# Kernel optimization log

Measured on AMD Instinct MI355X. Metric: run time of the kernel, lower is better.

Reference implementation:

```python
import jax, jax.numpy as jnp
import numpy as np

SPARSITY = 0.9  # target fraction of zeros (magnitude pruning)
D_IN = 4096
D_OUT = 4096
TOKENS = 4096


def setup_inputs() -> dict:
    key = jax.random.key(0)
    k1, k2 = jax.random.split(key)
    x = jax.random.normal(k1, (TOKENS, D_IN), dtype=jnp.float32)
    weight = jax.random.normal(k2, (D_OUT, D_IN), dtype=jnp.float32) * 0.01
    bias = jnp.zeros((D_OUT,), dtype=jnp.float32)
    return {"x": x, "weight": weight, "bias": bias}


def reference(x, weight, bias):
    # Magnitude pruning: threshold at the SPARSITY quantile of |W|,
    # keep only entries strictly above threshold (matches CSR build),
    # then sparse-dense GEMM y = x @ W_pruned^T + b.
    aw = jnp.abs(weight)
    thr = jnp.quantile(aw, SPARSITY)
    w_pruned = jnp.where(aw > thr, weight, jnp.zeros_like(weight))
    return x @ w_pruned.T + bias
```

## Files before the change

### kernel.cpp

```cpp
#include <hip/hip_runtime.h>
#include <stdint.h>

#define D_IN   4096
#define D_OUT  4096
#define NTOK   4096
#define NW     (D_OUT * D_IN)
#define RANK1  15099493u
#define CAP    1500000

typedef unsigned int  uint32;
typedef unsigned short ushort_t;
typedef float  f32x4  __attribute__((ext_vector_type(4)));
typedef __bf16 bf16x8 __attribute__((ext_vector_type(8)));

__device__ __forceinline__ uint32 rne_bf16(float f) {
  uint32 u = __float_as_uint(f);
  return (u + 0x7FFFu + ((u >> 16) & 1u)) >> 16;
}

__device__ __forceinline__ void gload_lds16(const void* g, void* l) {
  __builtin_amdgcn_global_load_lds((__attribute__((address_space(1))) void*)(g),
                                   (__attribute__((address_space(3))) void*)(l), 16, 0, 0);
}

template <int NB>
__device__ __forceinline__ void dsel(const uint32* __restrict__ h, uint32 rank,
                                     uint32* res, uint32* wtot) {
  constexpr int PER = NB >> 8;
  int tid = threadIdx.x;
  int lane = tid & 63, wid = tid >> 6;
  uint32 loc[PER];
  uint32 s = 0;
  int base = tid * PER;
#pragma unroll
  for (int i = 0; i < PER; i++) { loc[i] = h[base + i]; s += loc[i]; }
  uint32 v = s;
  for (int d = 1; d < 64; d <<= 1) { uint32 o = __shfl_up(v, (unsigned)d); if (lane >= d) v += o; }
  if (lane == 63) wtot[wid] = v;
  __syncthreads();
  uint32 woff = 0;
  for (int w = 0; w < wid; w++) woff += wtot[w];
  uint32 incl = v + woff, excl = incl - s;
  if (rank >= excl && rank < incl) {
    uint32 c = excl;
#pragma unroll
    for (int i = 0; i < PER; i++) {
      if (rank < c + loc[i]) { res[0] = (uint32)(base + i); res[1] = rank - c; break; }
      c += loc[i];
    }
  }
  __syncthreads();
}

__global__ void k1_hist1_convx(const uint4* __restrict__ wb, uint32* __restrict__ hist,
                               const float4* __restrict__ x, uint4* __restrict__ xout) {
  __shared__ uint32 lh[4][2048];
  if (blockIdx.x < 2048) {
    for (int i = threadIdx.x; i < 8192; i += 256) ((uint32*)lh)[i] = 0;
    __syncthreads();
    int wid = threadIdx.x >> 6;
    int idx = blockIdx.x * 256 + threadIdx.x;
    for (int i = idx; i < NW / 4; i += 2048 * 256) {
      uint4 v = wb[i];
      atomicAdd(&lh[wid][(v.x & 0x7FFFFFFFu) >> 20], 1u);
      atomicAdd(&lh[wid][(v.y & 0x7FFFFFFFu) >> 20], 1u);
      atomicAdd(&lh[wid][(v.z & 0x7FFFFFFFu) >> 20], 1u);
      atomicAdd(&lh[wid][(v.w & 0x7FFFFFFFu) >> 20], 1u);
    }
    __syncthreads();
    for (int i = threadIdx.x; i < 2048; i += 256) {
      uint32 c = lh[0][i] + lh[1][i] + lh[2][i] + lh[3][i];
      if (c) atomicAdd(&hist[i], c);
    }
  } else {
    int i = (blockIdx.x - 2048) * 256 + threadIdx.x;
    for (; i < NW / 8; i += 1024 * 256) {
      float4 a = x[2 * i], b = x[2 * i + 1];
      uint4 o;
      o.x = rne_bf16(a.x) | (rne_bf16(a.y) << 16);
      o.y = rne_bf16(a.z) | (rne_bf16(a.w) << 16);
      o.z = rne_bf16(b.x) | (rne_bf16(b.y) << 16);
      o.w = rne_bf16(b.z) | (rne_bf16(b.w) << 16);
      xout[i] = o;
    }
  }
}

__global__ void k2_decide(const float4* __restrict__ w, const uint32* __restrict__ hist1,
                          uint4* __restrict__ out, uint2* __restrict__ cand,
                          uint32* __restrict__ cnt) {
  __shared__ uint32 res1[2], wt[4];
  __shared__ uint32 lcnt, lbase;
  __shared__ uint2 lbuf[3072];
  if (threadIdx.x == 0) lcnt = 0;
  dsel<2048>(hist1, RANK1, res1, wt);
  uint32 bstar = res1[0];
  int i = blockIdx.x * 256 + threadIdx.x;
  for (; i < NW / 8; i += 512 * 256) {
    float4 a = w[2 * i], b = w[2 * i + 1];
    float f[8] = {a.x, a.y, a.z, a.w, b.x, b.y, b.z, b.w};
    uint32 h[8];
#pragma unroll
    for (int j = 0; j < 8; j++) {
      uint32 bits = __float_as_uint(f[j]);
      uint32 bin = (bits & 0x7FFFFFFFu) >> 20;
      h[j] = (bin > bstar) ? rne_bf16(f[j]) : 0u;
      if (bin == bstar) {
        uint32 p = atomicAdd(&lcnt, 1u);
        if (p < 3072) lbuf[p] = make_uint2((uint32)(8 * i + j), bits);
      }
    }
    uint4 o;
    o.x = h[0] | (h[1] << 16);
    o.y = h[2] | (h[3] << 16);
    o.z = h[4] | (h[5] << 16);
    o.w = h[6] | (h[7] << 16);
    out[i] = o;
  }
  __syncthreads();
  if (threadIdx.x == 0) lbase = atomicAdd(cnt, lcnt);
  __syncthreads();
  for (uint32 p = threadIdx.x; p < lcnt && p < 3072; p += 256) {
    uint32 g = lbase + p;
    if (g < CAP) cand[g] = lbuf[p];
  }
}

__global__ void s1_hist(const uint2* __restrict__ cand, const uint32* __restrict__ cnt,
                        uint32* __restrict__ hs1) {
  __shared__ uint32 lh[1024];
  for (int i = threadIdx.x; i < 1024; i += 256) lh[i] = 0;
  __syncthreads();
  uint32 n = *cnt; if (n > CAP) n = CAP;
  for (uint32 i = blockIdx.x * 256 + threadIdx.x; i < n; i += gridDim.x * 256) {
    uint32 mag = cand[i].y & 0x7FFFFFFFu;
    atomicAdd(&lh[(mag >> 10) & 1023u], 1u);
  }
  __syncthreads();
  for (int i = threadIdx.x; i < 1024; i += 256) if (lh[i]) atomicAdd(&hs1[i], lh[i]);
}

__global__ void s2_hist(const uint2* __restrict__ cand, const uint32* __restrict__ cnt,
                        const uint32* __restrict__ hist1, const uint32* __restrict__ hs1,
                        uint32* __restrict__ hs2) {
  __shared__ uint32 lh[1024];
  __shared__ uint32 res1[2], res2[2], wt[4];
  for (int i = threadIdx.x; i < 1024; i += 256) lh[i] = 0;
  dsel<2048>(hist1, RANK1, res1, wt);
  dsel<1024>(hs1, res1[1], res2, wt);
  uint32 b2 = res2[0];
  uint32 n = *cnt; if (n > CAP) n = CAP;
  for (uint32 i = blockIdx.x * 256 + threadIdx.x; i < n; i += gridDim.x * 256) {
    uint32 mag = cand[i].y & 0x7FFFFFFFu;
    if (((mag >> 10) & 1023u) == b2) atomicAdd(&lh[mag & 1023u], 1u);
  }
  __syncthreads();
  for (int i = threadIdx.x; i < 1024; i += 256) if (lh[i]) atomicAdd(&hs2[i], lh[i]);
}

__global__ void k5_fixup(const uint2* __restrict__ cand, const uint32* __restrict__ cnt,
                         const uint32* __restrict__ hist1, const uint32* __restrict__ hs1,
                         const uint32* __restrict__ hs2, ushort_t* __restrict__ wb) {
  __shared__ uint32 res1[2], res2[2], res3[2], wt[4];
  dsel<2048>(hist1, RANK1, res1, wt);
  dsel<1024>(hs1, res1[1], res2, wt);
  dsel<1024>(hs2, res2[1], res3, wt);
  uint32 thr_mag = (res1[0] << 20) | (res2[0] << 10) | res3[0];
  uint32 n = *cnt; if (n > CAP) n = CAP;
  for (uint32 i = blockIdx.x * 256 + threadIdx.x; i < n; i += gridDim.x * 256) {
    uint2 c = cand[i];
    uint32 mag = c.y & 0x7FFFFFFFu;
    if (mag > thr_mag) wb[c.x] = (ushort_t)rne_bf16(__uint_as_float(c.y));
  }
}

#define TILES 128

#define MF16(AF, BF, MO)                                                                          \
  acc[(MO)+0][0] = __builtin_amdgcn_mfma_f32_16x16x32_bf16(AF[0], BF[0], acc[(MO)+0][0], 0,0,0);  \
  acc[(MO)+0][1] = __builtin_amdgcn_mfma_f32_16x16x32_bf16(AF[0], BF[1], acc[(MO)+0][1], 0,0,0);  \
  acc[(MO)+0][2] = __builtin_amdgcn_mfma_f32_16x16x32_bf16(AF[0], BF[2], acc[(MO)+0][2], 0,0,0);  \
  acc[(MO)+0][3] = __builtin_amdgcn_mfma_f32_16x16x32_bf16(AF[0], BF[3], acc[(MO)+0][3], 0,0,0);  \
  acc[(MO)+1][0] = __builtin_amdgcn_mfma_f32_16x16x32_bf16(AF[1], BF[0], acc[(MO)+1][0], 0,0,0);  \
  acc[(MO)+1][1] = __builtin_amdgcn_mfma_f32_16x16x32_bf16(AF[1], BF[1], acc[(MO)+1][1], 0,0,0);  \
  acc[(MO)+1][2] = __builtin_amdgcn_mfma_f32_16x16x32_bf16(AF[1], BF[2], acc[(MO)+1][2], 0,0,0);  \
  acc[(MO)+1][3] = __builtin_amdgcn_mfma_f32_16x16x32_bf16(AF[1], BF[3], acc[(MO)+1][3], 0,0,0);  \
  acc[(MO)+2][0] = __builtin_amdgcn_mfma_f32_16x16x32_bf16(AF[2], BF[0], acc[(MO)+2][0], 0,0,0);  \
  acc[(MO)+2][1] = __builtin_amdgcn_mfma_f32_16x16x32_bf16(AF[2], BF[1], acc[(MO)+2][1], 0,0,0);  \
  acc[(MO)+2][2] = __builtin_amdgcn_mfma_f32_16x16x32_bf16(AF[2], BF[2], acc[(MO)+2][2], 0,0,0);  \
  acc[(MO)+2][3] = __builtin_amdgcn_mfma_f32_16x16x32_bf16(AF[2], BF[3], acc[(MO)+2][3], 0,0,0);  \
  acc[(MO)+3][0] = __builtin_amdgcn_mfma_f32_16x16x32_bf16(AF[3], BF[0], acc[(MO)+3][0], 0,0,0);  \
  acc[(MO)+3][1] = __builtin_amdgcn_mfma_f32_16x16x32_bf16(AF[3], BF[1], acc[(MO)+3][1], 0,0,0);  \
  acc[(MO)+3][2] = __builtin_amdgcn_mfma_f32_16x16x32_bf16(AF[3], BF[2], acc[(MO)+3][2], 0,0,0);  \
  acc[(MO)+3][3] = __builtin_amdgcn_mfma_f32_16x16x32_bf16(AF[3], BF[3], acc[(MO)+3][3], 0,0,0);

#define GBODY(T, S, SN)                                                        \
  {                                                                            \
    const bf16x8* A8n = (const bf16x8*)(lds + (((T) + 1) & 3) * 16384);        \
    const bf16x8* B8n = A8n + 1024;                                            \
    bv[SN][0]  = B8n[(br +  0) * 4 + csel];                                    \
    bv[SN][1]  = B8n[(br + 16) * 4 + csel];                                    \
    bv[SN][2]  = B8n[(br + 32) * 4 + csel];                                    \
    bv[SN][3]  = B8n[(br + 48) * 4 + csel];                                    \
    a03[SN][0] = A8n[(ar +  0) * 4 + csel];                                    \
    a03[SN][1] = A8n[(ar + 16) * 4 + csel];                                    \
    a03[SN][2] = A8n[(ar + 32) * 4 + csel];                                    \
    a03[SN][3] = A8n[(ar + 48) * 4 + csel];                                    \
    __builtin_amdgcn_sched_barrier(0);                                         \
    ushort_t* sb = lds + (((T) + 3) & 3) * 16384;                              \
    gload_lds16(pA0, sb + ld0);                                                \
    gload_lds16(pA1, sb + ld1);                                                \
    gload_lds16(pB0, sb + 8192 + ld0);                                         \
    gload_lds16(pB1, sb + 8192 + ld1);                                         \
    __builtin_amdgcn_sched_barrier(0);                                         \
    asm volatile("s_waitcnt lgkmcnt(8)" ::: "memory");                         \
    __builtin_amdgcn_sched_barrier(0);                                         \
    __builtin_amdgcn_s_setprio(1);                                             \
    MF16(a47[S], bv[S], 4)                                                     \
    __builtin_amdgcn_s_setprio(0);                                             \
    __builtin_amdgcn_sched_barrier(0);                                         \
    a47[SN][0] = A8n[(ar +  64) * 4 + csel];                                   \
    a47[SN][1] = A8n[(ar +  80) * 4 + csel];                                   \
    a47[SN][2] = A8n[(ar +  96) * 4 + csel];                                   \
    a47[SN][3] = A8n[(ar + 112) * 4 + csel];                                   \
    __builtin_amdgcn_sched_barrier(0);                                         \
    asm volatile("s_waitcnt lgkmcnt(4)" ::: "memory");                         \
    asm volatile("s_waitcnt vmcnt(4)" ::: "memory");                           \
    asm volatile("s_barrier" ::: "memory");                                    \
    __builtin_amdgcn_sched_barrier(0);                                         \
    __builtin_amdgcn_s_setprio(1);                                             \
    MF16(a03[SN], bv[SN], 0)                                                   \
    __builtin_amdgcn_s_setprio(0);                                             \
    __builtin_amdgcn_sched_barrier(0);                                         \
    if ((T) < TILES - 4) { pA0 += 32; pA1 += 32; pB0 += 32; pB1 += 32; }       \
  }

__global__ __launch_bounds__(512, 2) void gemm_bt(const ushort_t* __restrict__ A,
                                                  const ushort_t* __restrict__ B,
                                                  const float* __restrict__ bias,
                                                  float* __restrict__ C) {
  extern __shared__ ushort_t lds[];

  int bid = blockIdx.x;
  int swz = (bid & 7) * 32 + (bid >> 3);
  int bm = swz >> 4;
  int bn = swz & 15;

  int tid  = threadIdx.x;
  int lane = tid & 63;
  int wave = tid >> 6;
  int wm = wave >> 2, wn = wave & 3;

  int l15  = lane & 15;
  int csel = (lane >> 4) ^ ((lane >> 1) & 3);

  int idx0 = tid, idx1 = 512 + tid;
  int sr0 = idx0 >> 2, scl0 = (idx0 & 3) ^ ((sr0 >> 1) & 3);
  int sr1 = idx1 >> 2, scl1 = (idx1 & 3) ^ ((sr1 >> 1) & 3);
  int ld0 = idx0 * 8, ld1 = idx1 * 8;
  const ushort_t* pA0 = A + (size_t)(bm * 256 + sr0) * D_IN + scl0 * 8;
  const ushort_t* pA1 = A + (size_t)(bm * 256 + sr1) * D_IN + scl1 * 8;
  const ushort_t* pB0 = B + (size_t)(bn * 256 + sr0) * D_IN + scl0 * 8;
  const ushort_t* pB1 = B + (size_t)(bn * 256 + sr1) * D_IN + scl1 * 8;

  f32x4 acc[8][4];
#pragma unroll
  for (int m = 0; m < 8; m++)
#pragma unroll
    for (int n = 0; n < 4; n++) acc[m][n] = (f32x4){0.f, 0.f, 0.f, 0.f};

  gload_lds16(pA0,      lds + ld0);         gload_lds16(pA1,      lds + ld1);
  gload_lds16(pB0,      lds + 8192 + ld0);  gload_lds16(pB1,      lds + 8192 + ld1);
  gload_lds16(pA0 + 32, lds + 16384 + ld0); gload_lds16(pA1 + 32, lds + 16384 + ld1);
  gload_lds16(pB0 + 32, lds + 24576 + ld0); gload_lds16(pB1 + 32, lds + 24576 + ld1);
  gload_lds16(pA0 + 64, lds + 32768 + ld0); gload_lds16(pA1 + 64, lds + 32768 + ld1);
  gload_lds16(pB0 + 64, lds + 40960 + ld0); gload_lds16(pB1 + 64, lds + 40960 + ld1);
  pA0 += 96; pA1 += 96; pB0 += 96; pB1 += 96;
  asm volatile("s_waitcnt vmcnt(4)" ::: "memory");
  asm volatile("s_barrier" ::: "memory");

  int ar = wm * 128 + l15;
  int br = wn * 64 + l15;

  bf16x8 bv[2][4], a03[2][4], a47[2][4];

  {
    const bf16x8* A8 = (const bf16x8*)lds;
    const bf16x8* B8 = A8 + 1024;
    bv[0][0]  = B8[(br +  0) * 4 + csel];
    bv[0][1]  = B8[(br + 16) * 4 + csel];
    bv[0][2]  = B8[(br + 32) * 4 + csel];
    bv[0][3]  = B8[(br + 48) * 4 + csel];
    a03[0][0] = A8[(ar +  0) * 4 + csel];
    a03[0][1] = A8[(ar + 16) * 4 + csel];
    a03[0][2] = A8[(ar + 32) * 4 + csel];
    a03[0][3] = A8[(ar + 48) * 4 + csel];
    __builtin_amdgcn_sched_barrier(0);
    a47[0][0] = A8[(ar +  64) * 4 + csel];
    a47[0][1] = A8[(ar +  80) * 4 + csel];
    a47[0][2] = A8[(ar +  96) * 4 + csel];
    a47[0][3] = A8[(ar + 112) * 4 + csel];
    __builtin_amdgcn_sched_barrier(0);
    asm volatile("s_waitcnt lgkmcnt(4)" ::: "memory");
    __builtin_amdgcn_sched_barrier(0);
    __builtin_amdgcn_s_setprio(1);
    MF16(a03[0], bv[0], 0)
    __builtin_amdgcn_s_setprio(0);
    __builtin_amdgcn_sched_barrier(0);
  }

  for (int tt = 0; tt < 63; tt++) {
    int t0 = tt * 2;
    GBODY(t0, 0, 1)
    GBODY(t0 + 1, 1, 0)
  }
  GBODY(126, 0, 1)

  asm volatile("s_waitcnt lgkmcnt(0)" ::: "memory");
  __builtin_amdgcn_sched_barrier(0);
  __builtin_amdgcn_s_setprio(1);
  MF16(a47[1], bv[1], 4)
  __builtin_amdgcn_s_setprio(0);

  int orow0 = bm * 256 + wm * 128 + (lane >> 4) * 4;
  int ocol0 = bn * 256 + wn * 64 + l15;
#pragma unroll
  for (int n = 0; n < 4; n++) {
    float bb = bias[ocol0 + n * 16];
#pragma unroll
    for (int m = 0; m < 8; m++) {
#pragma unroll
      for (int r = 0; r < 4; r++) {
        C[(size_t)(orow0 + m * 16 + r) * D_OUT + ocol0 + n * 16] = acc[m][n][r] + bb;
      }
    }
  }
}

extern "C" void kernel_launch(void* const* d_in, const int* in_sizes, int n_in,
                              void* d_out, int out_size, void* d_ws, size_t ws_size,
                              hipStream_t stream) {
  const float* x = (const float*)d_in[0];
  const float* w = (const float*)d_in[1];
  const float* bias = (const float*)d_in[2];
  float* out = (float*)d_out;

  char* ws = (char*)d_ws;
  uint32* hist1 = (uint32*)ws;
  uint32* hs1   = (uint32*)(ws + 8192);
  uint32* hs2   = (uint32*)(ws + 12288);
  uint32* cnt   = (uint32*)(ws + 16384);
  ushort_t* Xb  = (ushort_t*)(ws + 65536);
  ushort_t* Wb  = (ushort_t*)(ws + 65536 + (size_t)NW * 2);
  uint2*   cand = (uint2*)(ws + 65536 + (size_t)NW * 4);

  hipMemsetAsync(d_ws, 0, 16448, stream);

  k1_hist1_convx<<<3072, 256, 0, stream>>>((const uint4*)w, hist1, (const float4*)x, (uint4*)Xb);
  k2_decide<<<512, 256, 0, stream>>>((const float4*)w, hist1, (uint4*)Wb, cand, cnt);
  s1_hist<<<128, 256, 0, stream>>>(cand, cnt, hs1);
  s2_hist<<<128, 256, 0, stream>>>(cand, cnt, hist1, hs1, hs2);
  k5_fixup<<<256, 256, 0, stream>>>(cand, cnt, hist1, hs1, hs2, Wb);

  gemm_bt<<<256, 512, 131072, stream>>>(Xb, Wb, bias, out);
}
```

Before: 212.5 us.

## Load B fragments directly from global into registers, stage only A in LDS

```diff
diff --git a/kernel.cpp b/kernel.cpp
--- a/kernel.cpp
+++ b/kernel.cpp
@@ -194,45 +194,51 @@
   acc[(MO)+3][2] = __builtin_amdgcn_mfma_f32_16x16x32_bf16(AF[3], BF[2], acc[(MO)+3][2], 0,0,0);  \
   acc[(MO)+3][3] = __builtin_amdgcn_mfma_f32_16x16x32_bf16(AF[3], BF[3], acc[(MO)+3][3], 0,0,0);
 
-#define GBODY(T, S, SN)                                                        \
+#define GBODY2(T, S, SN)                                                       \
   {                                                                            \
-    const bf16x8* A8n = (const bf16x8*)(lds + (((T) + 1) & 3) * 16384);        \
-    const bf16x8* B8n = A8n + 1024;                                            \
-    bv[SN][0]  = B8n[(br +  0) * 4 + csel];                                    \
-    bv[SN][1]  = B8n[(br + 16) * 4 + csel];                                    \
-    bv[SN][2]  = B8n[(br + 32) * 4 + csel];                                    \
-    bv[SN][3]  = B8n[(br + 48) * 4 + csel];                                    \
+                                     \
+    bq[SN][0] = *(const bf16x8*)pB0v;                                          \
+    bq[SN][1] = *(const bf16x8*)pB1v;                                          \
+    bq[SN][2] = *(const bf16x8*)pB2v;                                          \
+    bq[SN][3] = *(const bf16x8*)pB3v;                                          \
+    __builtin_amdgcn_sched_barrier(0);                                         \
+                                                  \
+    ushort_t* sb = lds + (((T) + 2) & 3) * 8192;                               \
+    gload_lds16(pA0, sb + ld0);                                                \
+    gload_lds16(pA1, sb + ld1);                                                \
+    __builtin_amdgcn_sched_barrier(0);                                         \
+                                                             \
+    const bf16x8* A8c = (const bf16x8*)(lds + ((T) & 3) * 8192);               \
+    a47[0] = A8c[(ar +  64) * 4 + csel];                                       \
+    a47[1] = A8c[(ar +  80) * 4 + csel];                                       \
+    a47[2] = A8c[(ar +  96) * 4 + csel];                                       \
+    a47[3] = A8c[(ar + 112) * 4 + csel];                                       \
+    __builtin_amdgcn_sched_barrier(0);                                         \
+    asm volatile("s_waitcnt lgkmcnt(4)" ::: "memory");      \
+    __builtin_amdgcn_sched_barrier(0);                                         \
+    __builtin_amdgcn_s_setprio(1);                                             \
+    MF16(a03[S], bq[S], 0)                                                     \
+    __builtin_amdgcn_s_setprio(0);                                             \
+    __builtin_amdgcn_sched_barrier(0);                                         \
+    asm volatile("s_waitcnt lgkmcnt(0)" ::: "memory");      \
+    __builtin_amdgcn_sched_barrier(0);                                         \
+    __builtin_amdgcn_s_setprio(1);                                             \
+    MF16(a47, bq[S], 4)                                                        \
+    __builtin_amdgcn_s_setprio(0);                                             \
+    __builtin_amdgcn_sched_barrier(0);                                         \
+                        \
+    asm volatile("s_waitcnt vmcnt(2)" ::: "memory");                           \
+    __builtin_amdgcn_sched_barrier(0);                                         \
+                                     \
+    const bf16x8* A8n = (const bf16x8*)(lds + (((T) + 1) & 3) * 8192);         \
     a03[SN][0] = A8n[(ar +  0) * 4 + csel];                                    \
     a03[SN][1] = A8n[(ar + 16) * 4 + csel];                                    \
     a03[SN][2] = A8n[(ar + 32) * 4 + csel];                                    \
     a03[SN][3] = A8n[(ar + 48) * 4 + csel];                                    \
     __builtin_amdgcn_sched_barrier(0);                                         \
-    ushort_t* sb = lds + (((T) + 3) & 3) * 16384;                              \
-    gload_lds16(pA0, sb + ld0);                                                \
-    gload_lds16(pA1, sb + ld1);                                                \
-    gload_lds16(pB0, sb + 8192 + ld0);                                         \
-    gload_lds16(pB1, sb + 8192 + ld1);                                         \
-    __builtin_amdgcn_sched_barrier(0);                                         \
-    asm volatile("s_waitcnt lgkmcnt(8)" ::: "memory");                         \
-    __builtin_amdgcn_sched_barrier(0);                                         \
-    __builtin_amdgcn_s_setprio(1);                                             \
-    MF16(a47[S], bv[S], 4)                                                     \
-    __builtin_amdgcn_s_setprio(0);                                             \
-    __builtin_amdgcn_sched_barrier(0);                                         \
-    a47[SN][0] = A8n[(ar +  64) * 4 + csel];                                   \
-    a47[SN][1] = A8n[(ar +  80) * 4 + csel];                                   \
-    a47[SN][2] = A8n[(ar +  96) * 4 + csel];                                   \
-    a47[SN][3] = A8n[(ar + 112) * 4 + csel];                                   \
-    __builtin_amdgcn_sched_barrier(0);                                         \
-    asm volatile("s_waitcnt lgkmcnt(4)" ::: "memory");                         \
-    asm volatile("s_waitcnt vmcnt(4)" ::: "memory");                           \
     asm volatile("s_barrier" ::: "memory");                                    \
-    __builtin_amdgcn_sched_barrier(0);                                         \
-    __builtin_amdgcn_s_setprio(1);                                             \
-    MF16(a03[SN], bv[SN], 0)                                                   \
-    __builtin_amdgcn_s_setprio(0);                                             \
-    __builtin_amdgcn_sched_barrier(0);                                         \
-    if ((T) < TILES - 4) { pA0 += 32; pA1 += 32; pB0 += 32; pB1 += 32; }       \
+    if ((T) < TILES - 3) { pA0 += 32; pA1 += 32; }                             \
+    if ((T) < TILES - 2) { pB0v += 32; pB1v += 32; pB2v += 32; pB3v += 32; }   \
   }
 
 __global__ __launch_bounds__(512, 2) void gemm_bt(const ushort_t* __restrict__ A,
@@ -252,7 +258,8 @@
   int wm = wave >> 2, wn = wave & 3;
 
   int l15  = lane & 15;
-  int csel = (lane >> 4) ^ ((lane >> 1) & 3);
+  int kq   = lane >> 4;
+  int csel = kq ^ ((lane >> 1) & 3);
 
   int idx0 = tid, idx1 = 512 + tid;
   int sr0 = idx0 >> 2, scl0 = (idx0 & 3) ^ ((sr0 >> 1) & 3);
@@ -260,8 +267,12 @@
   int ld0 = idx0 * 8, ld1 = idx1 * 8;
   const ushort_t* pA0 = A + (size_t)(bm * 256 + sr0) * D_IN + scl0 * 8;
   const ushort_t* pA1 = A + (size_t)(bm * 256 + sr1) * D_IN + scl1 * 8;
-  const ushort_t* pB0 = B + (size_t)(bn * 256 + sr0) * D_IN + scl0 * 8;
-  const ushort_t* pB1 = B + (size_t)(bn * 256 + sr1) * D_IN + scl1 * 8;
+
+  int brow = bn * 256 + wn * 64 + l15;
+  const ushort_t* pB0v = B + (size_t)(brow +  0) * D_IN + kq * 8 + 32;
+  const ushort_t* pB1v = B + (size_t)(brow + 16) * D_IN + kq * 8 + 32;
+  const ushort_t* pB2v = B + (size_t)(brow + 32) * D_IN + kq * 8 + 32;
+  const ushort_t* pB3v = B + (size_t)(brow + 48) * D_IN + kq * 8 + 32;
 
   f32x4 acc[8][4];
 #pragma unroll
@@ -269,58 +280,58 @@
 #pragma unroll
     for (int n = 0; n < 4; n++) acc[m][n] = (f32x4){0.f, 0.f, 0.f, 0.f};
 
-  gload_lds16(pA0,      lds + ld0);         gload_lds16(pA1,      lds + ld1);
-  gload_lds16(pB0,      lds + 8192 + ld0);  gload_lds16(pB1,      lds + 8192 + ld1);
-  gload_lds16(pA0 + 32, lds + 16384 + ld0); gload_lds16(pA1 + 32, lds + 16384 + ld1);
-  gload_lds16(pB0 + 32, lds + 24576 + ld0); gload_lds16(pB1 + 32, lds + 24576 + ld1);
-  gload_lds16(pA0 + 64, lds + 32768 + ld0); gload_lds16(pA1 + 64, lds + 32768 + ld1);
-  gload_lds16(pB0 + 64, lds + 40960 + ld0); gload_lds16(pB1 + 64, lds + 40960 + ld1);
-  pA0 += 96; pA1 += 96; pB0 += 96; pB1 += 96;
-  asm volatile("s_waitcnt vmcnt(4)" ::: "memory");
+  bf16x8 bq[2][4], a03[2][4], a47[4];
+
+  gload_lds16(pA0, lds + ld0);
+  gload_lds16(pA1, lds + ld1);
+  __builtin_amdgcn_sched_barrier(0);
+  bq[0][0] = *(const bf16x8*)(pB0v - 32);
+  bq[0][1] = *(const bf16x8*)(pB1v - 32);
+  bq[0][2] = *(const bf16x8*)(pB2v - 32);
+  bq[0][3] = *(const bf16x8*)(pB3v - 32);
+  __builtin_amdgcn_sched_barrier(0);
+  gload_lds16(pA0 + 32, lds + 8192 + ld0);
+  gload_lds16(pA1 + 32, lds + 8192 + ld1);
+  pA0 += 64; pA1 += 64;
+  __builtin_amdgcn_sched_barrier(0);
+  asm volatile("s_waitcnt vmcnt(2)" ::: "memory");
   asm volatile("s_barrier" ::: "memory");
 
   int ar = wm * 128 + l15;
-  int br = wn * 64 + l15;
-
-  bf16x8 bv[2][4], a03[2][4], a47[2][4];
 
   {
     const bf16x8* A8 = (const bf16x8*)lds;
-    const bf16x8* B8 = A8 + 1024;
-    bv[0][0]  = B8[(br +  0) * 4 + csel];
-    bv[0][1]  = B8[(br + 16) * 4 + csel];
-    bv[0][2]  = B8[(br + 32) * 4 + csel];
-    bv[0][3]  = B8[(br + 48) * 4 + csel];
     a03[0][0] = A8[(ar +  0) * 4 + csel];
     a03[0][1] = A8[(ar + 16) * 4 + csel];
     a03[0][2] = A8[(ar + 32) * 4 + csel];
     a03[0][3] = A8[(ar + 48) * 4 + csel];
     __builtin_amdgcn_sched_barrier(0);
-    a47[0][0] = A8[(ar +  64) * 4 + csel];
-    a47[0][1] = A8[(ar +  80) * 4 + csel];
-    a47[0][2] = A8[(ar +  96) * 4 + csel];
-    a47[0][3] = A8[(ar + 112) * 4 + csel];
+  }
+
+  for (int tt = 0; tt < 63; tt++) {
+    GBODY2(2 * tt,     0, 1)
+    GBODY2(2 * tt + 1, 1, 0)
+  }
+  GBODY2(126, 0, 1)
+
+  {
+    const bf16x8* A8c = (const bf16x8*)(lds + (127 & 3) * 8192);
+    a47[0] = A8c[(ar +  64) * 4 + csel];
+    a47[1] = A8c[(ar +  80) * 4 + csel];
+    a47[2] = A8c[(ar +  96) * 4 + csel];
+    a47[3] = A8c[(ar + 112) * 4 + csel];
     __builtin_amdgcn_sched_barrier(0);
     asm volatile("s_waitcnt lgkmcnt(4)" ::: "memory");
     __builtin_amdgcn_sched_barrier(0);
     __builtin_amdgcn_s_setprio(1);
-    MF16(a03[0], bv[0], 0)
+    MF16(a03[1], bq[1], 0)
     __builtin_amdgcn_s_setprio(0);
+    asm volatile("s_waitcnt lgkmcnt(0)" ::: "memory");
     __builtin_amdgcn_sched_barrier(0);
-  }
-
-  for (int tt = 0; tt < 63; tt++) {
-    int t0 = tt * 2;
-    GBODY(t0, 0, 1)
-    GBODY(t0 + 1, 1, 0)
-  }
-  GBODY(126, 0, 1)
-
-  asm volatile("s_waitcnt lgkmcnt(0)" ::: "memory");
-  __builtin_amdgcn_sched_barrier(0);
-  __builtin_amdgcn_s_setprio(1);
-  MF16(a47[1], bv[1], 4)
-  __builtin_amdgcn_s_setprio(0);
+    __builtin_amdgcn_s_setprio(1);
+    MF16(a47, bq[1], 4)
+    __builtin_amdgcn_s_setprio(0);
+  }
 
   int orow0 = bm * 256 + wm * 128 + (lane >> 4) * 4;
   int ocol0 = bn * 256 + wn * 64 + l15;
@@ -362,5 +373,5 @@
   s2_hist<<<128, 256, 0, stream>>>(cand, cnt, hist1, hs1, hs2);
   k5_fixup<<<256, 256, 0, stream>>>(cand, cnt, hist1, hs1, hs2, Wb);
 
-  gemm_bt<<<256, 512, 131072, stream>>>(Xb, Wb, bias, out);
-}
+  gemm_bt<<<256, 512, 65536, stream>>>(Xb, Wb, bias, out);
+}
```

Result: slower. 293.0 us (+37.9%).

## Fuse pruning prep kernels into one persistent kernel with grid barriers

Applied to the files above, without the earlier changes.

```diff
diff --git a/kernel.cpp b/kernel.cpp
--- a/kernel.cpp
+++ b/kernel.cpp
@@ -7,6 +7,7 @@
 #define NW     (D_OUT * D_IN)
 #define RANK1  15099493u
 #define CAP    1500000
+#define PREPB  1024
 
 typedef unsigned int  uint32;
 typedef unsigned short ushort_t;
@@ -23,9 +24,21 @@
                                    (__attribute__((address_space(3))) void*)(l), 16, 0, 0);
 }
 
+__device__ __forceinline__ void gridbar(uint32* bar, uint32 target) {
+  __syncthreads();
+  __threadfence();
+  if (threadIdx.x == 0) {
+    __hip_atomic_fetch_add(bar, 1u, __ATOMIC_RELAXED, __HIP_MEMORY_SCOPE_AGENT);
+    while (__hip_atomic_load(bar, __ATOMIC_RELAXED, __HIP_MEMORY_SCOPE_AGENT) < target)
+      __builtin_amdgcn_s_sleep(8);
+  }
+  __syncthreads();
+  __threadfence();
+}
+
 template <int NB>
 __device__ __forceinline__ void dsel(const uint32* __restrict__ h, uint32 rank,
-                                     uint32* res, uint32* wtot) {
+                                     volatile uint32* res, volatile uint32* wtot) {
   constexpr int PER = NB >> 8;
   int tid = threadIdx.x;
   int lane = tid & 63, wid = tid >> 6;
@@ -52,29 +65,34 @@
   __syncthreads();
 }
 
-__global__ void k1_hist1_convx(const uint4* __restrict__ wb, uint32* __restrict__ hist,
-                               const float4* __restrict__ x, uint4* __restrict__ xout) {
-  __shared__ uint32 lh[4][2048];
-  if (blockIdx.x < 2048) {
-    for (int i = threadIdx.x; i < 8192; i += 256) ((uint32*)lh)[i] = 0;
-    __syncthreads();
-    int wid = threadIdx.x >> 6;
-    int idx = blockIdx.x * 256 + threadIdx.x;
-    for (int i = idx; i < NW / 4; i += 2048 * 256) {
-      uint4 v = wb[i];
-      atomicAdd(&lh[wid][(v.x & 0x7FFFFFFFu) >> 20], 1u);
-      atomicAdd(&lh[wid][(v.y & 0x7FFFFFFFu) >> 20], 1u);
-      atomicAdd(&lh[wid][(v.z & 0x7FFFFFFFu) >> 20], 1u);
-      atomicAdd(&lh[wid][(v.w & 0x7FFFFFFFu) >> 20], 1u);
-    }
-    __syncthreads();
-    for (int i = threadIdx.x; i < 2048; i += 256) {
-      uint32 c = lh[0][i] + lh[1][i] + lh[2][i] + lh[3][i];
-      if (c) atomicAdd(&hist[i], c);
-    }
-  } else {
-    int i = (blockIdx.x - 2048) * 256 + threadIdx.x;
-    for (; i < NW / 8; i += 1024 * 256) {
+__global__ __launch_bounds__(256, 4) void prep(const float* __restrict__ w,
+                                               const float4* __restrict__ x,
+                                               uint4* __restrict__ xout,
+                                               uint4* __restrict__ wout,
+                                               uint2* __restrict__ cand,
+                                               uint32* __restrict__ hist1,
+                                               uint32* __restrict__ hs1,
+                                               uint32* __restrict__ hs2,
+                                               uint32* __restrict__ cnt,
+                                               uint32* __restrict__ bar) {
+  __shared__ uint32 smem[8192];
+  __shared__ uint32 sres1[2], sres2[2], sres3[2], swt[4], slcnt, slbase;
+  int tid = threadIdx.x, bid = blockIdx.x;
+
+  {
+    uint32* lh = smem;
+    for (int i = tid; i < 8192; i += 256) lh[i] = 0;
+    __syncthreads();
+    int wid = tid >> 6;
+    const uint4* wb4 = (const uint4*)w;
+    for (int i = bid * 256 + tid; i < NW / 4; i += PREPB * 256) {
+      uint4 v = wb4[i];
+      atomicAdd(&lh[wid * 2048 + ((v.x & 0x7FFFFFFFu) >> 20)], 1u);
+      atomicAdd(&lh[wid * 2048 + ((v.y & 0x7FFFFFFFu) >> 20)], 1u);
+      atomicAdd(&lh[wid * 2048 + ((v.z & 0x7FFFFFFFu) >> 20)], 1u);
+      atomicAdd(&lh[wid * 2048 + ((v.w & 0x7FFFFFFFu) >> 20)], 1u);
+    }
+    for (int i = bid * 256 + tid; i < NW / 8; i += PREPB * 256) {
       float4 a = x[2 * i], b = x[2 * i + 1];
       uint4 o;
       o.x = rne_bf16(a.x) | (rne_bf16(a.y) << 16);
@@ -83,94 +101,85 @@
       o.w = rne_bf16(b.z) | (rne_bf16(b.w) << 16);
       xout[i] = o;
     }
-  }
-}
-
-__global__ void k2_decide(const float4* __restrict__ w, const uint32* __restrict__ hist1,
-                          uint4* __restrict__ out, uint2* __restrict__ cand,
-                          uint32* __restrict__ cnt) {
-  __shared__ uint32 res1[2], wt[4];
-  __shared__ uint32 lcnt, lbase;
-  __shared__ uint2 lbuf[3072];
-  if (threadIdx.x == 0) lcnt = 0;
-  dsel<2048>(hist1, RANK1, res1, wt);
-  uint32 bstar = res1[0];
-  int i = blockIdx.x * 256 + threadIdx.x;
-  for (; i < NW / 8; i += 512 * 256) {
-    float4 a = w[2 * i], b = w[2 * i + 1];
-    float f[8] = {a.x, a.y, a.z, a.w, b.x, b.y, b.z, b.w};
-    uint32 h[8];
-#pragma unroll
-    for (int j = 0; j < 8; j++) {
-      uint32 bits = __float_as_uint(f[j]);
-      uint32 bin = (bits & 0x7FFFFFFFu) >> 20;
-      h[j] = (bin > bstar) ? rne_bf16(f[j]) : 0u;
-      if (bin == bstar) {
-        uint32 p = atomicAdd(&lcnt, 1u);
-        if (p < 3072) lbuf[p] = make_uint2((uint32)(8 * i + j), bits);
+    __syncthreads();
+    for (int i = tid; i < 2048; i += 256) {
+      uint32 c = lh[i] + lh[2048 + i] + lh[4096 + i] + lh[6144 + i];
+      if (c) atomicAdd(&hist1[i], c);
+    }
+  }
+  gridbar(bar, PREPB);
+
+  {
+    uint2*  lbuf = (uint2*)smem;
+    uint32* lch  = smem + 6144;
+    for (int i = tid; i < 1024; i += 256) lch[i] = 0;
+    if (tid == 0) slcnt = 0;
+    dsel<2048>(hist1, RANK1, sres1, swt);
+    uint32 bstar = sres1[0];
+    const float4* w4 = (const float4*)w;
+    for (int i = bid * 256 + tid; i < NW / 8; i += PREPB * 256) {
+      float4 a = w4[2 * i], b = w4[2 * i + 1];
+      float f[8] = {a.x, a.y, a.z, a.w, b.x, b.y, b.z, b.w};
+      uint32 h[8];
+#pragma unroll
+      for (int j = 0; j < 8; j++) {
+        uint32 bits = __float_as_uint(f[j]);
+        uint32 bin = (bits & 0x7FFFFFFFu) >> 20;
+        h[j] = (bin > bstar) ? rne_bf16(f[j]) : 0u;
+        if (bin == bstar) {
+          uint32 p = atomicAdd(&slcnt, 1u);
+          if (p < 3072) {
+            lbuf[p] = make_uint2((uint32)(8 * i + j), bits);
+            atomicAdd(&lch[(bits >> 10) & 1023u], 1u);
+          }
+        }
       }
-    }
-    uint4 o;
-    o.x = h[0] | (h[1] << 16);
-    o.y = h[2] | (h[3] << 16);
-    o.z = h[4] | (h[5] << 16);
-    o.w = h[6] | (h[7] << 16);
-    out[i] = o;
-  }
-  __syncthreads();
-  if (threadIdx.x == 0) lbase = atomicAdd(cnt, lcnt);
-  __syncthreads();
-  for (uint32 p = threadIdx.x; p < lcnt && p < 3072; p += 256) {
-    uint32 g = lbase + p;
-    if (g < CAP) cand[g] = lbuf[p];
-  }
-}
-
-__global__ void s1_hist(const uint2* __restrict__ cand, const uint32* __restrict__ cnt,
-                        uint32* __restrict__ hs1) {
-  __shared__ uint32 lh[1024];
-  for (int i = threadIdx.x; i < 1024; i += 256) lh[i] = 0;
-  __syncthreads();
-  uint32 n = *cnt; if (n > CAP) n = CAP;
-  for (uint32 i = blockIdx.x * 256 + threadIdx.x; i < n; i += gridDim.x * 256) {
-    uint32 mag = cand[i].y & 0x7FFFFFFFu;
-    atomicAdd(&lh[(mag >> 10) & 1023u], 1u);
-  }
-  __syncthreads();
-  for (int i = threadIdx.x; i < 1024; i += 256) if (lh[i]) atomicAdd(&hs1[i], lh[i]);
-}
-
-__global__ void s2_hist(const uint2* __restrict__ cand, const uint32* __restrict__ cnt,
-                        const uint32* __restrict__ hist1, const uint32* __restrict__ hs1,
-                        uint32* __restrict__ hs2) {
-  __shared__ uint32 lh[1024];
-  __shared__ uint32 res1[2], res2[2], wt[4];
-  for (int i = threadIdx.x; i < 1024; i += 256) lh[i] = 0;
-  dsel<2048>(hist1, RANK1, res1, wt);
-  dsel<1024>(hs1, res1[1], res2, wt);
-  uint32 b2 = res2[0];
-  uint32 n = *cnt; if (n > CAP) n = CAP;
-  for (uint32 i = blockIdx.x * 256 + threadIdx.x; i < n; i += gridDim.x * 256) {
-    uint32 mag = cand[i].y & 0x7FFFFFFFu;
-    if (((mag >> 10) & 1023u) == b2) atomicAdd(&lh[mag & 1023u], 1u);
-  }
-  __syncthreads();
-  for (int i = threadIdx.x; i < 1024; i += 256) if (lh[i]) atomicAdd(&hs2[i], lh[i]);
-}
-
-__global__ void k5_fixup(const uint2* __restrict__ cand, const uint32* __restrict__ cnt,
-                         const uint32* __restrict__ hist1, const uint32* __restrict__ hs1,
-                         const uint32* __restrict__ hs2, ushort_t* __restrict__ wb) {
-  __shared__ uint32 res1[2], res2[2], res3[2], wt[4];
-  dsel<2048>(hist1, RANK1, res1, wt);
-  dsel<1024>(hs1, res1[1], res2, wt);
-  dsel<1024>(hs2, res2[1], res3, wt);
-  uint32 thr_mag = (res1[0] << 20) | (res2[0] << 10) | res3[0];
-  uint32 n = *cnt; if (n > CAP) n = CAP;
-  for (uint32 i = blockIdx.x * 256 + threadIdx.x; i < n; i += gridDim.x * 256) {
-    uint2 c = cand[i];
-    uint32 mag = c.y & 0x7FFFFFFFu;
-    if (mag > thr_mag) wb[c.x] = (ushort_t)rne_bf16(__uint_as_float(c.y));
+      uint4 o;
+      o.x = h[0] | (h[1] << 16);
+      o.y = h[2] | (h[3] << 16);
+      o.z = h[4] | (h[5] << 16);
+      o.w = h[6] | (h[7] << 16);
+      wout[i] = o;
+    }
+    __syncthreads();
+    uint32 nstore = slcnt < 3072u ? slcnt : 3072u;
+    if (tid == 0) slbase = atomicAdd(cnt, nstore);
+    __syncthreads();
+    for (uint32 p = tid; p < nstore; p += 256) {
+      uint32 g = slbase + p;
+      if (g < CAP) cand[g] = lbuf[p];
+    }
+    for (int i = tid; i < 1024; i += 256) if (lch[i]) atomicAdd(&hs1[i], lch[i]);
+  }
+  gridbar(bar, 2 * PREPB);
+
+  {
+    for (int i = tid; i < 1024; i += 256) smem[i] = 0;
+    dsel<2048>(hist1, RANK1, sres1, swt);
+    dsel<1024>(hs1, sres1[1], sres2, swt);
+    uint32 b2 = sres2[0];
+    uint32 n = *cnt; if (n > CAP) n = CAP;
+    for (uint32 i = bid * 256 + tid; i < n; i += PREPB * 256) {
+      uint32 mag = cand[i].y & 0x7FFFFFFFu;
+      if (((mag >> 10) & 1023u) == b2) atomicAdd(&smem[mag & 1023u], 1u);
+    }
+    __syncthreads();
+    for (int i = tid; i < 1024; i += 256) if (smem[i]) atomicAdd(&hs2[i], smem[i]);
+  }
+  gridbar(bar, 3 * PREPB);
+
+  {
+    dsel<2048>(hist1, RANK1, sres1, swt);
+    dsel<1024>(hs1, sres1[1], sres2, swt);
+    dsel<1024>(hs2, sres2[1], sres3, swt);
+    uint32 thr_mag = (sres1[0] << 20) | (sres2[0] << 10) | sres3[0];
+    uint32 n = *cnt; if (n > CAP) n = CAP;
+    ushort_t* wb16 = (ushort_t*)wout;
+    for (uint32 i = bid * 256 + tid; i < n; i += PREPB * 256) {
+      uint2 c = cand[i];
+      uint32 mag = c.y & 0x7FFFFFFFu;
+      if (mag > thr_mag) wb16[c.x] = (ushort_t)rne_bf16(__uint_as_float(c.y));
+    }
   }
 }
 
@@ -350,17 +359,15 @@
   uint32* hs1   = (uint32*)(ws + 8192);
   uint32* hs2   = (uint32*)(ws + 12288);
   uint32* cnt   = (uint32*)(ws + 16384);
+  uint32* bar   = (uint32*)(ws + 16388);
   ushort_t* Xb  = (ushort_t*)(ws + 65536);
   ushort_t* Wb  = (ushort_t*)(ws + 65536 + (size_t)NW * 2);
   uint2*   cand = (uint2*)(ws + 65536 + (size_t)NW * 4);
 
   hipMemsetAsync(d_ws, 0, 16448, stream);
 
-  k1_hist1_convx<<<3072, 256, 0, stream>>>((const uint4*)w, hist1, (const float4*)x, (uint4*)Xb);
-  k2_decide<<<512, 256, 0, stream>>>((const float4*)w, hist1, (uint4*)Wb, cand, cnt);
-  s1_hist<<<128, 256, 0, stream>>>(cand, cnt, hs1);
-  s2_hist<<<128, 256, 0, stream>>>(cand, cnt, hist1, hs1, hs2);
-  k5_fixup<<<256, 256, 0, stream>>>(cand, cnt, hist1, hs1, hs2, Wb);
+  prep<<<PREPB, 256, 0, stream>>>(w, (const float4*)x, (uint4*)Xb, (uint4*)Wb,
+                                  cand, hist1, hs1, hs2, cnt, bar);
 
   gemm_bt<<<256, 512, 131072, stream>>>(Xb, Wb, bias, out);
 }
```

Result: slower. 778.0 us (+266.1%).

## Fuse candidate histogram into decide kernel and restructure GEMM as paired-tile double buffer

Applied to the files above, without the earlier changes.

```diff
diff --git a/kernel.cpp b/kernel.cpp
--- a/kernel.cpp
+++ b/kernel.cpp
@@ -88,10 +88,12 @@
 
 __global__ void k2_decide(const float4* __restrict__ w, const uint32* __restrict__ hist1,
                           uint4* __restrict__ out, uint2* __restrict__ cand,
-                          uint32* __restrict__ cnt) {
+                          uint32* __restrict__ cnt, uint32* __restrict__ hs1) {
   __shared__ uint32 res1[2], wt[4];
   __shared__ uint32 lcnt, lbase;
   __shared__ uint2 lbuf[3072];
+  __shared__ uint32 lch[1024];
+  for (int i = threadIdx.x; i < 1024; i += 256) lch[i] = 0;
   if (threadIdx.x == 0) lcnt = 0;
   dsel<2048>(hist1, RANK1, res1, wt);
   uint32 bstar = res1[0];
@@ -107,7 +109,10 @@
       h[j] = (bin > bstar) ? rne_bf16(f[j]) : 0u;
       if (bin == bstar) {
         uint32 p = atomicAdd(&lcnt, 1u);
-        if (p < 3072) lbuf[p] = make_uint2((uint32)(8 * i + j), bits);
+        if (p < 3072) {
+          lbuf[p] = make_uint2((uint32)(8 * i + j), bits);
+          atomicAdd(&lch[(bits >> 10) & 1023u], 1u);
+        }
       }
     }
     uint4 o;
@@ -118,26 +123,14 @@
     out[i] = o;
   }
   __syncthreads();
-  if (threadIdx.x == 0) lbase = atomicAdd(cnt, lcnt);
-  __syncthreads();
-  for (uint32 p = threadIdx.x; p < lcnt && p < 3072; p += 256) {
+  uint32 nstore = lcnt < 3072u ? lcnt : 3072u;
+  if (threadIdx.x == 0) lbase = atomicAdd(cnt, nstore);
+  __syncthreads();
+  for (uint32 p = threadIdx.x; p < nstore; p += 256) {
     uint32 g = lbase + p;
     if (g < CAP) cand[g] = lbuf[p];
   }
-}
-
-__global__ void s1_hist(const uint2* __restrict__ cand, const uint32* __restrict__ cnt,
-                        uint32* __restrict__ hs1) {
-  __shared__ uint32 lh[1024];
-  for (int i = threadIdx.x; i < 1024; i += 256) lh[i] = 0;
-  __syncthreads();
-  uint32 n = *cnt; if (n > CAP) n = CAP;
-  for (uint32 i = blockIdx.x * 256 + threadIdx.x; i < n; i += gridDim.x * 256) {
-    uint32 mag = cand[i].y & 0x7FFFFFFFu;
-    atomicAdd(&lh[(mag >> 10) & 1023u], 1u);
-  }
-  __syncthreads();
-  for (int i = threadIdx.x; i < 1024; i += 256) if (lh[i]) atomicAdd(&hs1[i], lh[i]);
+  for (int ii = threadIdx.x; ii < 1024; ii += 256) if (lch[ii]) atomicAdd(&hs1[ii], lch[ii]);
 }
 
 __global__ void s2_hist(const uint2* __restrict__ cand, const uint32* __restrict__ cnt,
@@ -194,45 +187,76 @@
   acc[(MO)+3][2] = __builtin_amdgcn_mfma_f32_16x16x32_bf16(AF[3], BF[2], acc[(MO)+3][2], 0,0,0);  \
   acc[(MO)+3][3] = __builtin_amdgcn_mfma_f32_16x16x32_bf16(AF[3], BF[3], acc[(MO)+3][3], 0,0,0);
 
-#define GBODY(T, S, SN)                                                        \
+#define SUPER(BE, BO, SE, SO, ADV)                                             \
   {                                                                            \
-    const bf16x8* A8n = (const bf16x8*)(lds + (((T) + 1) & 3) * 16384);        \
-    const bf16x8* B8n = A8n + 1024;                                            \
-    bv[SN][0]  = B8n[(br +  0) * 4 + csel];                                    \
-    bv[SN][1]  = B8n[(br + 16) * 4 + csel];                                    \
-    bv[SN][2]  = B8n[(br + 32) * 4 + csel];                                    \
-    bv[SN][3]  = B8n[(br + 48) * 4 + csel];                                    \
-    a03[SN][0] = A8n[(ar +  0) * 4 + csel];                                    \
-    a03[SN][1] = A8n[(ar + 16) * 4 + csel];                                    \
-    a03[SN][2] = A8n[(ar + 32) * 4 + csel];                                    \
-    a03[SN][3] = A8n[(ar + 48) * 4 + csel];                                    \
-    __builtin_amdgcn_sched_barrier(0);                                         \
-    ushort_t* sb = lds + (((T) + 3) & 3) * 16384;                              \
-    gload_lds16(pA0, sb + ld0);                                                \
-    gload_lds16(pA1, sb + ld1);                                                \
-    gload_lds16(pB0, sb + 8192 + ld0);                                         \
-    gload_lds16(pB1, sb + 8192 + ld1);                                         \
+    asm volatile("s_barrier" ::: "memory");                                    \
+    gload_lds16(pA0,      lds + (SE) * 16384 + ld0);                           \
+    gload_lds16(pA1,      lds + (SE) * 16384 + ld1);                           \
+    gload_lds16(pB0,      lds + (SE) * 16384 + 8192 + ld0);                    \
+    gload_lds16(pB1,      lds + (SE) * 16384 + 8192 + ld1);                    \
+    gload_lds16(pA0 + 32, lds + (SO) * 16384 + ld0);                           \
+    gload_lds16(pA1 + 32, lds + (SO) * 16384 + ld1);                           \
+    gload_lds16(pB0 + 32, lds + (SO) * 16384 + 8192 + ld0);                    \
+    gload_lds16(pB1 + 32, lds + (SO) * 16384 + 8192 + ld1);                    \
+    __builtin_amdgcn_sched_barrier(0);                                         \
+    const bf16x8* A8e = (const bf16x8*)(lds + (BE) * 16384);                   \
+    const bf16x8* B8e = A8e + 1024;                                            \
+    const bf16x8* A8o = (const bf16x8*)(lds + (BO) * 16384);                   \
+    const bf16x8* B8o = A8o + 1024;                                            \
+    bvE[0]  = B8e[(br +  0) * 4 + csel];                                       \
+    bvE[1]  = B8e[(br + 16) * 4 + csel];                                       \
+    bvE[2]  = B8e[(br + 32) * 4 + csel];                                       \
+    bvE[3]  = B8e[(br + 48) * 4 + csel];                                       \
+    a03E[0] = A8e[(ar +  0) * 4 + csel];                                       \
+    a03E[1] = A8e[(ar + 16) * 4 + csel];                                       \
+    a03E[2] = A8e[(ar + 32) * 4 + csel];                                       \
+    a03E[3] = A8e[(ar + 48) * 4 + csel];                                       \
+    __builtin_amdgcn_sched_barrier(0);                                         \
+    a47E[0] = A8e[(ar +  64) * 4 + csel];                                      \
+    a47E[1] = A8e[(ar +  80) * 4 + csel];                                      \
+    a47E[2] = A8e[(ar +  96) * 4 + csel];                                      \
+    a47E[3] = A8e[(ar + 112) * 4 + csel];                                      \
+    __builtin_amdgcn_sched_barrier(0);                                         \
+    asm volatile("s_waitcnt lgkmcnt(4)" ::: "memory");                         \
+    __builtin_amdgcn_sched_barrier(0);                                         \
+    __builtin_amdgcn_s_setprio(1);                                             \
+    MF16(a03E, bvE, 0)                                                         \
+    __builtin_amdgcn_s_setprio(0);                                             \
+    __builtin_amdgcn_sched_barrier(0);                                         \
+    bvO[0]  = B8o[(br +  0) * 4 + csel];                                       \
+    bvO[1]  = B8o[(br + 16) * 4 + csel];                                       \
+    bvO[2]  = B8o[(br + 32) * 4 + csel];                                       \
+    bvO[3]  = B8o[(br + 48) * 4 + csel];                                       \
+    a03O[0] = A8o[(ar +  0) * 4 + csel];                                       \
+    a03O[1] = A8o[(ar + 16) * 4 + csel];                                       \
+    a03O[2] = A8o[(ar + 32) * 4 + csel];                                       \
+    a03O[3] = A8o[(ar + 48) * 4 + csel];                                       \
     __builtin_amdgcn_sched_barrier(0);                                         \
     asm volatile("s_waitcnt lgkmcnt(8)" ::: "memory");                         \
     __builtin_amdgcn_sched_barrier(0);                                         \
     __builtin_amdgcn_s_setprio(1);                                             \
-    MF16(a47[S], bv[S], 4)                                                     \
+    MF16(a47E, bvE, 4)                                                         \
     __builtin_amdgcn_s_setprio(0);                                             \
     __builtin_amdgcn_sched_barrier(0);                                         \
-    a47[SN][0] = A8n[(ar +  64) * 4 + csel];                                   \
-    a47[SN][1] = A8n[(ar +  80) * 4 + csel];                                   \
-    a47[SN][2] = A8n[(ar +  96) * 4 + csel];                                   \
-    a47[SN][3] = A8n[(ar + 112) * 4 + csel];                                   \
+    a47O[0] = A8o[(ar +  64) * 4 + csel];                                      \
+    a47O[1] = A8o[(ar +  80) * 4 + csel];                                      \
+    a47O[2] = A8o[(ar +  96) * 4 + csel];                                      \
+    a47O[3] = A8o[(ar + 112) * 4 + csel];                                      \
     __builtin_amdgcn_sched_barrier(0);                                         \
     asm volatile("s_waitcnt lgkmcnt(4)" ::: "memory");                         \
-    asm volatile("s_waitcnt vmcnt(4)" ::: "memory");                           \
-    asm volatile("s_barrier" ::: "memory");                                    \
     __builtin_amdgcn_sched_barrier(0);                                         \
     __builtin_amdgcn_s_setprio(1);                                             \
-    MF16(a03[SN], bv[SN], 0)                                                   \
+    MF16(a03O, bvO, 0)                                                         \
     __builtin_amdgcn_s_setprio(0);                                             \
     __builtin_amdgcn_sched_barrier(0);                                         \
-    if ((T) < TILES - 4) { pA0 += 32; pA1 += 32; pB0 += 32; pB1 += 32; }       \
+    asm volatile("s_waitcnt lgkmcnt(0)" ::: "memory");                         \
+    __builtin_amdgcn_sched_barrier(0);                                         \
+    __builtin_amdgcn_s_setprio(1);                                             \
+    MF16(a47O, bvO, 4)                                                         \
+    __builtin_amdgcn_s_setprio(0);                                             \
+    __builtin_amdgcn_sched_barrier(0);                                         \
+    asm volatile("s_waitcnt vmcnt(0)" ::: "memory");                           \
+    if (ADV) { pA0 += 64; pA1 += 64; pB0 += 64; pB1 += 64; }                   \
   }
 
 __global__ __launch_bounds__(512, 2) void gemm_bt(const ushort_t* __restrict__ A,
@@ -269,58 +293,27 @@
 #pragma unroll
     for (int n = 0; n < 4; n++) acc[m][n] = (f32x4){0.f, 0.f, 0.f, 0.f};
 
-  gload_lds16(pA0,      lds + ld0);         gload_lds16(pA1,      lds + ld1);
-  gload_lds16(pB0,      lds + 8192 + ld0);  gload_lds16(pB1,      lds + 8192 + ld1);
-  gload_lds16(pA0 + 32, lds + 16384 + ld0); gload_lds16(pA1 + 32, lds + 16384 + ld1);
-  gload_lds16(pB0 + 32, lds + 24576 + ld0); gload_lds16(pB1 + 32, lds + 24576 + ld1);
-  gload_lds16(pA0 + 64, lds + 32768 + ld0); gload_lds16(pA1 + 64, lds + 32768 + ld1);
-  gload_lds16(pB0 + 64, lds + 40960 + ld0); gload_lds16(pB1 + 64, lds + 40960 + ld1);
-  pA0 += 96; pA1 += 96; pB0 += 96; pB1 += 96;
-  asm volatile("s_waitcnt vmcnt(4)" ::: "memory");
-  asm volatile("s_barrier" ::: "memory");
+  gload_lds16(pA0,      lds + ld0);
+  gload_lds16(pA1,      lds + ld1);
+  gload_lds16(pB0,      lds + 8192 + ld0);
+  gload_lds16(pB1,      lds + 8192 + ld1);
+  gload_lds16(pA0 + 32, lds + 16384 + ld0);
+  gload_lds16(pA1 + 32, lds + 16384 + ld1);
+  gload_lds16(pB0 + 32, lds + 16384 + 8192 + ld0);
+  gload_lds16(pB1 + 32, lds + 16384 + 8192 + ld1);
+  pA0 += 64; pA1 += 64; pB0 += 64; pB1 += 64;
+  asm volatile("s_waitcnt vmcnt(0)" ::: "memory");
 
   int ar = wm * 128 + l15;
   int br = wn * 64 + l15;
 
-  bf16x8 bv[2][4], a03[2][4], a47[2][4];
-
-  {
-    const bf16x8* A8 = (const bf16x8*)lds;
-    const bf16x8* B8 = A8 + 1024;
-    bv[0][0]  = B8[(br +  0) * 4 + csel];
-    bv[0][1]  = B8[(br + 16) * 4 + csel];
-    bv[0][2]  = B8[(br + 32) * 4 + csel];
-    bv[0][3]  = B8[(br + 48) * 4 + csel];
-    a03[0][0] = A8[(ar +  0) * 4 + csel];
-    a03[0][1] = A8[(ar + 16) * 4 + csel];
-    a03[0][2] = A8[(ar + 32) * 4 + csel];
-    a03[0][3] = A8[(ar + 48) * 4 + csel];
-    __builtin_amdgcn_sched_barrier(0);
-    a47[0][0] = A8[(ar +  64) * 4 + csel];
-    a47[0][1] = A8[(ar +  80) * 4 + csel];
-    a47[0][2] = A8[(ar +  96) * 4 + csel];
-    a47[0][3] = A8[(ar + 112) * 4 + csel];
-    __builtin_amdgcn_sched_barrier(0);
-    asm volatile("s_waitcnt lgkmcnt(4)" ::: "memory");
-    __builtin_amdgcn_sched_barrier(0);
-    __builtin_amdgcn_s_setprio(1);
-    MF16(a03[0], bv[0], 0)
-    __builtin_amdgcn_s_setprio(0);
-    __builtin_amdgcn_sched_barrier(0);
-  }
-
-  for (int tt = 0; tt < 63; tt++) {
-    int t0 = tt * 2;
-    GBODY(t0, 0, 1)
-    GBODY(t0 + 1, 1, 0)
-  }
-  GBODY(126, 0, 1)
-
-  asm volatile("s_waitcnt lgkmcnt(0)" ::: "memory");
-  __builtin_amdgcn_sched_barrier(0);
-  __builtin_amdgcn_s_setprio(1);
-  MF16(a47[1], bv[1], 4)
-  __builtin_amdgcn_s_setprio(0);
+  bf16x8 bvE[4], a03E[4], a47E[4], bvO[4], a03O[4], a47O[4];
+
+  for (int kk = 0; kk < 32; kk++) {
+    bool adv = kk < 31;
+    SUPER(0, 1, 2, 3, true)
+    SUPER(2, 3, 0, 1, adv)
+  }
 
   int orow0 = bm * 256 + wm * 128 + (lane >> 4) * 4;
   int ocol0 = bn * 256 + wn * 64 + l15;
@@ -357,8 +350,7 @@
   hipMemsetAsync(d_ws, 0, 16448, stream);
 
   k1_hist1_convx<<<3072, 256, 0, stream>>>((const uint4*)w, hist1, (const float4*)x, (uint4*)Xb);
-  k2_decide<<<512, 256, 0, stream>>>((const float4*)w, hist1, (uint4*)Wb, cand, cnt);
-  s1_hist<<<128, 256, 0, stream>>>(cand, cnt, hs1);
+  k2_decide<<<512, 256, 0, stream>>>((const float4*)w, hist1, (uint4*)Wb, cand, cnt, hs1);
   s2_hist<<<128, 256, 0, stream>>>(cand, cnt, hist1, hs1, hs2);
   k5_fixup<<<256, 256, 0, stream>>>(cand, cnt, hist1, hs1, hs2, Wb);
 
```

Result: slower. 224.2 us (+5.5%).
